# Kernel tuning notes

Measured on AMD Instinct MI355X. Metric: run time of the kernel, lower is better.

Reference implementation:

```python
import jax, jax.numpy as jnp
import numpy as np

NEG_INF = -1000000000.0
B, S, E, H = 2, 2048, 1024, 16
HD = E // H


def setup_inputs() -> dict:
    key = jax.random.key(0)
    ks = jax.random.split(key, 5)
    sd = 1.0 / np.sqrt(E)
    return {
        "x": jax.random.normal(ks[0], (B, S, E), dtype=jnp.float32),
        "Wqkv": jax.random.normal(ks[1], (3 * E, E), dtype=jnp.float32) * sd,
        "bqkv": jax.random.normal(ks[2], (3 * E,), dtype=jnp.float32) * sd,
        "Wout": jax.random.normal(ks[3], (E, E), dtype=jnp.float32) * sd,
        "bout": jax.random.normal(ks[4], (E,), dtype=jnp.float32) * sd,
    }


def reference(x, Wqkv, bqkv, Wout, bout):
    # qkv projection (torch Linear: x @ W.T + b)
    qkv = x @ Wqkv.T + bqkv                      # [B, S, 3E]
    qkv = qkv.reshape(B, S, H, 3 * HD).transpose(0, 2, 1, 3)  # [B, H, S, 3*hd]
    q, k, v = jnp.split(qkv, 3, axis=-1)          # each [B, H, S, hd]
    scaled = jnp.einsum('bhqd,bhkd->bhqk', q, k) / jnp.sqrt(jnp.float32(HD))
    # faithful to source: mask = tril(ones) * NEG_INF (lower triangle incl. diagonal gets -1e9)
    mask = jnp.tril(jnp.ones((S, S), dtype=jnp.float32)) * NEG_INF
    scaled = scaled + mask                        # broadcast over [B, H]
    attention = jax.nn.softmax(scaled, axis=-1)
    values = jnp.einsum('bhqk,bhkd->bhqd', attention, v)
    values = values.transpose(0, 2, 1, 3).reshape(B, S, E)
    out = values @ Wout.T + bout
    return out
```

## Files before the change

kernel.cpp:

```cpp
#include <hip/hip_runtime.h>
#include <hip/hip_bf16.h>
#include <math.h>

#define Bb 2
#define Ss 2048
#define Ee 1024
#define Hh 16
#define HDd 64
#define NEG_INF_F -1000000000.0f

typedef __attribute__((ext_vector_type(8))) short bfrag;
typedef __attribute__((ext_vector_type(4))) float ffrag;
typedef __attribute__((ext_vector_type(16))) float ffrag16;
typedef __attribute__((ext_vector_type(8))) unsigned short us8;

#define C1F 0.1803368801f

__device__ __forceinline__ unsigned short f2bf(float x) {
  unsigned u = __float_as_uint(x);
  u += 0x7fffu + ((u >> 16) & 1u);
  return (unsigned short)(u >> 16);
}
__device__ __forceinline__ float bf2f(unsigned short h) {
  return __uint_as_float(((unsigned)h) << 16);
}

__device__ __forceinline__ void async_copy16(void* lds, const void* g) {
  __builtin_amdgcn_global_load_lds(
      (const __attribute__((address_space(1))) unsigned int*)g,
      (__attribute__((address_space(3))) unsigned int*)lds, 16, 0, 0);
}

__global__ __launch_bounds__(256) void split_all(
    const float* __restrict__ x, unsigned short* __restrict__ xh,
    const float* __restrict__ wq, unsigned short* __restrict__ wqh,
    unsigned short* __restrict__ wql,
    const float* __restrict__ wo, unsigned short* __restrict__ woh,
    unsigned short* __restrict__ wol) {
  int bid = blockIdx.x;
  const float* in;
  unsigned short *hi, *lo;
  if (bid < 4096) { in = x; hi = xh; lo = nullptr; }
  else if (bid < 7168) { bid -= 4096; in = wq; hi = wqh; lo = wql; }
  else { bid -= 7168; in = wo; hi = woh; lo = wol; }
  const int idx = (bid * 256 + threadIdx.x) * 4;
  const float4 v = *(const float4*)(in + idx);
  unsigned short h0 = f2bf(v.x), h1 = f2bf(v.y), h2 = f2bf(v.z), h3 = f2bf(v.w);
  ushort4 hv = {h0, h1, h2, h3};
  *(ushort4*)(hi + idx) = hv;
  if (lo) {
    ushort4 lv = {f2bf(v.x - bf2f(h0)), f2bf(v.y - bf2f(h1)),
                  f2bf(v.z - bf2f(h2)), f2bf(v.w - bf2f(h3))};
    *(ushort4*)(lo + idx) = lv;
  }
}

__device__ __forceinline__ int gemm_slot(int row, int q) {
  return (row >> 1) * 8 + ((((row & 1) * 4) | q) ^ ((row >> 1) & 7));
}
__device__ __forceinline__ int slot_src_off(int slot, int ld) {
  const int dr = slot >> 3;
  const int idx8 = (slot & 7) ^ (dr & 7);
  const int row = dr * 2 + (idx8 >> 2);
  const int q = idx8 & 3;
  return row * ld + q * 8;
}

__global__ __launch_bounds__(256) void gemm_qkv(
    const unsigned short* __restrict__ Ah,
    const unsigned short* __restrict__ Bh, const unsigned short* __restrict__ Bl,
    const float* __restrict__ bias,
    unsigned short* __restrict__ q_h, unsigned short* __restrict__ k_h,
    unsigned short* __restrict__ vt_h) {
  __shared__ unsigned short sm[3 * 4096];
  const int tid = threadIdx.x;
  const int lane = tid & 63;
  const int w = tid >> 6;
  const int wm = w >> 1;
  const int wn = w & 1;
  const int l31 = lane & 31;
  const int e = lane >> 5;
  const int m0 = blockIdx.x * 128;
  const int n0 = blockIdx.y * 128;

  int coff[2], ldsb[2];
#pragma unroll
  for (int u = 0; u < 2; ++u) {
    const int slot = w * 128 + u * 64 + lane;
    coff[u] = slot_src_off(slot, 1024);
    ldsb[u] = (w * 128 + u * 64) * 8;
  }
  const unsigned short* srcs[3] = {
      Ah + (size_t)m0 * 1024, Bh + (size_t)n0 * 1024, Bl + (size_t)n0 * 1024};

  ffrag16 acc[2][2];
#pragma unroll
  for (int i = 0; i < 2; ++i)
#pragma unroll
    for (int j = 0; j < 2; ++j) acc[i][j] = (ffrag16)0.f;

  int ca[2][2], cb[2][2];
#pragma unroll
  for (int t = 0; t < 2; ++t)
#pragma unroll
    for (int h2 = 0; h2 < 2; ++h2) {
      ca[t][h2] = gemm_slot(wm * 64 + t * 32 + l31, h2 * 2 + e) * 8;
      cb[t][h2] = gemm_slot(wn * 64 + t * 32 + l31, h2 * 2 + e) * 8;
    }

  for (int k0 = 0; k0 < 1024; k0 += 32) {
    __syncthreads();
#pragma unroll
    for (int t = 0; t < 3; ++t)
#pragma unroll
      for (int u = 0; u < 2; ++u)
        async_copy16(&sm[t * 4096 + ldsb[u]], srcs[t] + coff[u] + k0);
    __syncthreads();

    bfrag ah[2][2], bhf[2][2], blf[2][2];
#pragma unroll
    for (int t = 0; t < 2; ++t)
#pragma unroll
      for (int h2 = 0; h2 < 2; ++h2) {
        ah[t][h2] = *(const bfrag*)&sm[0 * 4096 + ca[t][h2]];
        bhf[t][h2] = *(const bfrag*)&sm[1 * 4096 + cb[t][h2]];
        blf[t][h2] = *(const bfrag*)&sm[2 * 4096 + cb[t][h2]];
      }
#pragma unroll
    for (int mt = 0; mt < 2; ++mt)
#pragma unroll
      for (int nt = 0; nt < 2; ++nt)
#pragma unroll
        for (int h2 = 0; h2 < 2; ++h2) {
          acc[mt][nt] = __builtin_amdgcn_mfma_f32_32x32x16_bf16(
              ah[mt][h2], bhf[nt][h2], acc[mt][nt], 0, 0, 0);
          acc[mt][nt] = __builtin_amdgcn_mfma_f32_32x32x16_bf16(
              ah[mt][h2], blf[nt][h2], acc[mt][nt], 0, 0, 0);
        }
  }

#pragma unroll
  for (int nt = 0; nt < 2; ++nt) {
    const int n = n0 + wn * 64 + nt * 32 + l31;
    const float bv = bias[n];
    const int h = n / 192;
    const int c = n - h * 192;
    const int d = c & 63;
#pragma unroll
    for (int mt = 0; mt < 2; ++mt) {
      if (c >= 128) {
#pragma unroll
        for (int g = 0; g < 4; ++g) {
          const int m = m0 + wm * 64 + mt * 32 + g * 8 + e * 4;
          const int bidx = m >> 11;
          const int s = m & 2047;
          ushort4 hv4;
          unsigned short* ph = (unsigned short*)&hv4;
#pragma unroll
          for (int r = 0; r < 4; ++r)
            ph[r] = f2bf(acc[mt][nt][g * 4 + r] + bv);
          const size_t off =
              (size_t)(bidx * 16 + h) * (64 * 2048) + (size_t)d * 2048 + s;
          *(ushort4*)(vt_h + off) = hv4;
        }
      } else {
        const float scale = (c < 64) ? C1F : 1.0f;
        unsigned short* dh = (c < 64) ? q_h : k_h;
#pragma unroll
        for (int g = 0; g < 4; ++g)
#pragma unroll
          for (int r = 0; r < 4; ++r) {
            const int m = m0 + wm * 64 + mt * 32 + g * 8 + e * 4 + r;
            const int bidx = m >> 11;
            const int s = m & 2047;
            const size_t off =
                (size_t)(bidx * 16 + h) * (2048 * 64) + (size_t)s * 64 + d;
            dh[off] = f2bf((acc[mt][nt][g * 4 + r] + bv) * scale);
          }
      }
    }
  }
}

__global__ __launch_bounds__(256) void gemm_out2(
    const unsigned short* __restrict__ A,
    const unsigned short* __restrict__ Bh, const unsigned short* __restrict__ Bl,
    const float* __restrict__ bias, float* __restrict__ out) {
  __shared__ unsigned short sm[8192];
  const int tid = threadIdx.x;
  const int lane = tid & 63;
  const int w = tid >> 6;
  const int wm = w >> 1;
  const int wn = w & 1;
  const int l31 = lane & 31;
  const int e = lane >> 5;
  const int m0 = blockIdx.x * 128;
  const int n0 = blockIdx.y * 64;

  int acoff[2], aldsb[2];
#pragma unroll
  for (int u = 0; u < 2; ++u) {
    const int slot = w * 128 + u * 64 + lane;
    acoff[u] = slot_src_off(slot, 1024);
    aldsb[u] = (w * 128 + u * 64) * 8;
  }
  const int bslot = w * 64 + lane;
  const int bcoff = slot_src_off(bslot, 1024);
  const int bldsb = bslot * 8;

  const unsigned short* Ap  = A + (size_t)m0 * 1024;
  const unsigned short* Bph = Bh + (size_t)n0 * 1024;
  const unsigned short* Bpl = Bl + (size_t)n0 * 1024;

  ffrag16 acc[2];
  acc[0] = (ffrag16)0.f;
  acc[1] = (ffrag16)0.f;

  int ca[2][2], cb[2];
#pragma unroll
  for (int t = 0; t < 2; ++t)
#pragma unroll
    for (int h2 = 0; h2 < 2; ++h2)
      ca[t][h2] = gemm_slot(wm * 64 + t * 32 + l31, h2 * 2 + e) * 8;
#pragma unroll
  for (int h2 = 0; h2 < 2; ++h2)
    cb[h2] = gemm_slot(wn * 32 + l31, h2 * 2 + e) * 8;

  for (int k0 = 0; k0 < 1024; k0 += 32) {
    __syncthreads();
#pragma unroll
    for (int u = 0; u < 2; ++u)
      async_copy16(&sm[0 + aldsb[u]], Ap + acoff[u] + k0);
    async_copy16(&sm[4096 + bldsb], Bph + bcoff + k0);
    async_copy16(&sm[6144 + bldsb], Bpl + bcoff + k0);
    __syncthreads();

    bfrag ah[2][2], bhf[2], blf[2];
#pragma unroll
    for (int t = 0; t < 2; ++t)
#pragma unroll
      for (int h2 = 0; h2 < 2; ++h2)
        ah[t][h2] = *(const bfrag*)&sm[0 + ca[t][h2]];
#pragma unroll
    for (int h2 = 0; h2 < 2; ++h2) {
      bhf[h2] = *(const bfrag*)&sm[4096 + cb[h2]];
      blf[h2] = *(const bfrag*)&sm[6144 + cb[h2]];
    }
#pragma unroll
    for (int mt = 0; mt < 2; ++mt)
#pragma unroll
      for (int h2 = 0; h2 < 2; ++h2) {
        acc[mt] = __builtin_amdgcn_mfma_f32_32x32x16_bf16(
            ah[mt][h2], bhf[h2], acc[mt], 0, 0, 0);
        acc[mt] = __builtin_amdgcn_mfma_f32_32x32x16_bf16(
            ah[mt][h2], blf[h2], acc[mt], 0, 0, 0);
      }
  }

  const int n = n0 + wn * 32 + l31;
  const float bv = bias[n];
#pragma unroll
  for (int mt = 0; mt < 2; ++mt)
#pragma unroll
    for (int g = 0; g < 4; ++g)
#pragma unroll
      for (int r = 0; r < 4; ++r) {
        const int m = m0 + wm * 64 + mt * 32 + g * 8 + e * 4 + r;
        out[(size_t)m * 1024 + n] = acc[mt][g * 4 + r] + bv;
      }
}

__global__ __launch_bounds__(256, 4) void attn_2ph(
    const unsigned short* __restrict__ qh, const unsigned short* __restrict__ kh,
    const unsigned short* __restrict__ vth, unsigned short* __restrict__ vals) {
  __shared__ unsigned short sm[2 * 8192 + 4096];
  const int tid = threadIdx.x;
  const int lane = tid & 63;
  const int w = tid >> 6;
  const int l15 = lane & 15;
  const int quad = lane >> 4;
  const int bh = blockIdx.x;
  const int y = blockIdx.y;
  const size_t base = (size_t)bh * (Ss * HDd);
  const int b = bh >> 4;
  const int h = bh & 15;
  const int PB = 16384;

  const int c0 = w * 128 + lane;
  const int c1 = c0 + 64;
  const int r0 = c0 >> 3, r1 = c1 >> 3;
  const int s0 = ((c0 & 7) ^ (r0 & 7)) * 8;
  const int s1 = ((c1 & 7) ^ (r1 & 7)) * 8;
  const int koff0 = r0 * 64 + s0, koff1 = r1 * 64 + s1;
  const int voff0 = r0 * 2048 + s0, voff1 = r1 * 2048 + s1;
  const int ldsc0 = c0 * 8;
  const int ldsc1 = c1 * 8;

  bfrag vone;
#pragma unroll
  for (int j = 0; j < 8; ++j) vone[j] = (short)0x3F80;

  const bool fixw = (y == 0) && (w == 3);
  ffrag Vsum[4];
#pragma unroll
  for (int dt = 0; dt < 4; ++dt) Vsum[dt] = (ffrag)0.f;

  for (int ph = 0; ph < 2; ++ph) {
    const int ybk = ph ? (31 - y) : y;
    const int rb = 64 * ybk + 16 * w;

    bfrag Qf[2];
#pragma unroll
    for (int ks = 0; ks < 2; ++ks)
      Qf[ks] = *(const bfrag*)(qh + base + (size_t)(rb + l15) * 64 + ks * 32 + quad * 8);

    ffrag O[4], Oe;
#pragma unroll
    for (int dt = 0; dt < 4; ++dt) O[dt] = (ffrag)0.f;
    Oe = (ffrag)0.f;

    int cur = 0, nxt = 8192;
    {
      const unsigned short* kp = kh + base + ybk * 4096;
      const unsigned short* vp = vth + base + ybk * 64;
      async_copy16(&sm[cur + ldsc0], kp + koff0);
      async_copy16(&sm[cur + ldsc1], kp + koff1);
      async_copy16(&sm[cur + 4096 + ldsc0], vp + voff0);
      async_copy16(&sm[cur + 4096 + ldsc1], vp + voff1);
    }

    for (int kt = ybk; kt < 32; ++kt) {
      __syncthreads();
      if (kt + 1 < 32) {
        const unsigned short* kp = kh + base + (kt + 1) * 4096;
        const unsigned short* vp = vth + base + (kt + 1) * 64;
        async_copy16(&sm[nxt + ldsc0], kp + koff0);
        async_copy16(&sm[nxt + ldsc1], kp + koff1);
        async_copy16(&sm[nxt + 4096 + ldsc0], vp + voff0);
        async_copy16(&sm[nxt + 4096 + ldsc1], vp + voff1);
      }

      ffrag S[4];
#pragma unroll
      for (int nt = 0; nt < 4; ++nt) S[nt] = (ffrag)0.f;
#pragma unroll
      for (int nt = 0; nt < 4; ++nt) {
        const int krow = nt * 16 + l15;
#pragma unroll
        for (int ks = 0; ks < 2; ++ks) {
          const bfrag kbh =
              *(const bfrag*)&sm[cur + krow * 64 + ((ks * 4 + quad) ^ (krow & 7)) * 8];
          S[nt] = __builtin_amdgcn_mfma_f32_16x16x32_bf16(Qf[ks], kbh, S[nt], 0, 0, 0);
        }
      }

      const float CM = -1.442695041e9f;
      const bool partial = (kt == ybk);
#pragma unroll
      for (int nt = 0; nt < 4; ++nt) {
        const int key = nt * 16 + l15;
#pragma unroll
        for (int rp = 0; rp < 2; ++rp) {
          float t0 = S[nt][2 * rp];
          float t1 = S[nt][2 * rp + 1];
          if (partial) {
            const int jg = kt * 64 + key;
            const int ig = rb + quad * 4 + 2 * rp;
            if (jg <= ig) t0 += CM;
            if (jg <= ig + 1) t1 += CM;
          }
          float2 pf;
          pf.x = __builtin_amdgcn_exp2f(t0);
          pf.y = __builtin_amdgcn_exp2f(t1);
          const __hip_bfloat162 pb = __float22bfloat162_rn(pf);
          const unsigned short* pbs = (const unsigned short*)&pb;
          const int pr0 = w * 16 + quad * 4 + 2 * rp;
          sm[PB + pr0 * 64 + (((key >> 3) ^ (pr0 & 7)) * 8 + (key & 7))] = pbs[0];
          const int pr1 = pr0 + 1;
          sm[PB + pr1 * 64 + (((key >> 3) ^ (pr1 & 7)) * 8 + (key & 7))] = pbs[1];
        }
      }

#pragma unroll
      for (int ks = 0; ks < 2; ++ks) {
        const int prow = w * 16 + l15;
        const bfrag pA =
            *(const bfrag*)&sm[PB + prow * 64 + ((ks * 4 + quad) ^ (prow & 7)) * 8];
        Oe = __builtin_amdgcn_mfma_f32_16x16x32_bf16(pA, vone, Oe, 0, 0, 0);
#pragma unroll
        for (int dt = 0; dt < 4; ++dt) {
          const int vrow = dt * 16 + l15;
          const bfrag vbh =
              *(const bfrag*)&sm[cur + 4096 + vrow * 64 + ((ks * 4 + quad) ^ (vrow & 7)) * 8];
          O[dt] = __builtin_amdgcn_mfma_f32_16x16x32_bf16(pA, vbh, O[dt], 0, 0, 0);
          if (fixw && ph == 0)
            Vsum[dt] = __builtin_amdgcn_mfma_f32_16x16x32_bf16(vone, vbh, Vsum[dt], 0, 0, 0);
        }
      }
      const int t = cur; cur = nxt; nxt = t;
    }

#pragma unroll
    for (int r = 0; r < 4; ++r) {
      const float inv = 1.0f / Oe[r];
      const int s = rb + quad * 4 + r;
      const size_t rowoff = ((size_t)b * 2048 + s) * 1024 + h * 64;
#pragma unroll
      for (int dt = 0; dt < 4; ++dt) {
        float val = O[dt][r] * inv;
        if (fixw && ph == 1 && quad == 3 && r == 3)
          val = Vsum[dt][3] * (1.0f / 2048.0f);
        vals[rowoff + dt * 16 + l15] = f2bf(val);
      }
    }
    __syncthreads();
  }
}

extern "C" void kernel_launch(void* const* d_in, const int* in_sizes, int n_in,
                              void* d_out, int out_size, void* d_ws, size_t ws_size,
                              hipStream_t stream) {
  const float* x    = (const float*)d_in[0];
  const float* Wqkv = (const float*)d_in[1];
  const float* bqkv = (const float*)d_in[2];
  const float* Wout = (const float*)d_in[3];
  const float* bout = (const float*)d_in[4];
  float* out = (float*)d_out;
  char* wsb = (char*)d_ws;

  unsigned short* qhp  = (unsigned short*)d_ws;
  unsigned short* khp  = qhp + 1 * 4194304;
  unsigned short* vthp = qhp + 2 * 4194304;
  unsigned short* vals = qhp + 3 * 4194304;
  unsigned short* wqh  = (unsigned short*)(wsb + (48u << 20));
  unsigned short* wql  = (unsigned short*)(wsb + (54u << 20));
  unsigned short* woh  = (unsigned short*)(wsb + (60u << 20));
  unsigned short* wol  = (unsigned short*)(wsb + (62u << 20));
  unsigned short* xh   = (unsigned short*)d_out;

  dim3 blk(256);
  split_all<<<8192, blk, 0, stream>>>(x, xh, Wqkv, wqh, wql, Wout, woh, wol);
  gemm_qkv<<<dim3(32, 24), blk, 0, stream>>>(xh, wqh, wql, bqkv, qhp, khp, vthp);
  attn_2ph<<<dim3(32, 16), blk, 0, stream>>>(qhp, khp, vthp, vals);
  gemm_out2<<<dim3(32, 16), blk, 0, stream>>>(vals, woh, wol, bout, out);
}
```

Baseline: 202.6 us.

## Triple-buffer LDS in QKV and output GEMMs with async prefetch two tiles ahead

Replaces the load-then-sync loop in both projection GEMMs with a three-stage LDS ring buffer. Global-to-LDS async copies are issued two K-steps ahead and waited on with explicit vmcnt waitcnts plus a single barrier per step. This overlaps global memory latency with MFMA work and drops one of the two barriers per iteration. It triples shared memory per block, which can lower occupancy, and it relies on hand-coded waitcnt encodings matching the number of copies in flight.

```diff
diff --git a/kernel.cpp b/kernel.cpp
--- a/kernel.cpp
+++ b/kernel.cpp
@@ -15,6 +15,10 @@
 typedef __attribute__((ext_vector_type(8))) unsigned short us8;
 
 #define C1F 0.1803368801f
+
+#define WAIT_VM6 0x0F76
+#define WAIT_VM4 0x0F74
+#define WAIT_VM0 0x0F70
 
 __device__ __forceinline__ unsigned short f2bf(float x) {
   unsigned u = __float_as_uint(x);
@@ -72,7 +76,7 @@
     const float* __restrict__ bias,
     unsigned short* __restrict__ q_h, unsigned short* __restrict__ k_h,
     unsigned short* __restrict__ vt_h) {
-  __shared__ unsigned short sm[3 * 4096];
+  __shared__ unsigned short sm[3 * 12288];
   const int tid = threadIdx.x;
   const int lane = tid & 63;
   const int w = tid >> 6;
@@ -108,23 +112,40 @@
       cb[t][h2] = gemm_slot(wn * 64 + t * 32 + l31, h2 * 2 + e) * 8;
     }
 
-  for (int k0 = 0; k0 < 1024; k0 += 32) {
-    __syncthreads();
-#pragma unroll
-    for (int t = 0; t < 3; ++t)
-#pragma unroll
-      for (int u = 0; u < 2; ++u)
-        async_copy16(&sm[t * 4096 + ldsb[u]], srcs[t] + coff[u] + k0);
-    __syncthreads();
+#pragma unroll
+  for (int t = 0; t < 3; ++t)
+#pragma unroll
+    for (int u = 0; u < 2; ++u)
+      async_copy16(&sm[0 + t * 4096 + ldsb[u]], srcs[t] + coff[u] + 0);
+#pragma unroll
+  for (int t = 0; t < 3; ++t)
+#pragma unroll
+    for (int u = 0; u < 2; ++u)
+      async_copy16(&sm[12288 + t * 4096 + ldsb[u]], srcs[t] + coff[u] + 32);
+
+  int b0 = 0, b1 = 12288, b2 = 24576;
+  for (int k = 0; k < 32; ++k) {
+    if (k < 31) __builtin_amdgcn_s_waitcnt(WAIT_VM6);
+    else        __builtin_amdgcn_s_waitcnt(WAIT_VM0);
+    __builtin_amdgcn_s_barrier();
+    __builtin_amdgcn_sched_barrier(0);
+    if (k + 2 < 32) {
+      const int k0 = (k + 2) * 32;
+#pragma unroll
+      for (int t = 0; t < 3; ++t)
+#pragma unroll
+        for (int u = 0; u < 2; ++u)
+          async_copy16(&sm[b2 + t * 4096 + ldsb[u]], srcs[t] + coff[u] + k0);
+    }
 
     bfrag ah[2][2], bhf[2][2], blf[2][2];
 #pragma unroll
     for (int t = 0; t < 2; ++t)
 #pragma unroll
       for (int h2 = 0; h2 < 2; ++h2) {
-        ah[t][h2] = *(const bfrag*)&sm[0 * 4096 + ca[t][h2]];
-        bhf[t][h2] = *(const bfrag*)&sm[1 * 4096 + cb[t][h2]];
-        blf[t][h2] = *(const bfrag*)&sm[2 * 4096 + cb[t][h2]];
+        ah[t][h2] = *(const bfrag*)&sm[b0 + 0 + ca[t][h2]];
+        bhf[t][h2] = *(const bfrag*)&sm[b0 + 4096 + cb[t][h2]];
+        blf[t][h2] = *(const bfrag*)&sm[b0 + 8192 + cb[t][h2]];
       }
 #pragma unroll
     for (int mt = 0; mt < 2; ++mt)
@@ -137,6 +158,7 @@
           acc[mt][nt] = __builtin_amdgcn_mfma_f32_32x32x16_bf16(
               ah[mt][h2], blf[nt][h2], acc[mt][nt], 0, 0, 0);
         }
+    const int tb = b0; b0 = b1; b1 = b2; b2 = tb;
   }
 
 #pragma unroll
@@ -186,7 +208,7 @@
     const unsigned short* __restrict__ A,
     const unsigned short* __restrict__ Bh, const unsigned short* __restrict__ Bl,
     const float* __restrict__ bias, float* __restrict__ out) {
-  __shared__ unsigned short sm[8192];
+  __shared__ unsigned short sm[3 * 8192];
   const int tid = threadIdx.x;
   const int lane = tid & 63;
   const int w = tid >> 6;
@@ -226,25 +248,44 @@
   for (int h2 = 0; h2 < 2; ++h2)
     cb[h2] = gemm_slot(wn * 32 + l31, h2 * 2 + e) * 8;
 
-  for (int k0 = 0; k0 < 1024; k0 += 32) {
-    __syncthreads();
+  {
 #pragma unroll
     for (int u = 0; u < 2; ++u)
-      async_copy16(&sm[0 + aldsb[u]], Ap + acoff[u] + k0);
-    async_copy16(&sm[4096 + bldsb], Bph + bcoff + k0);
-    async_copy16(&sm[6144 + bldsb], Bpl + bcoff + k0);
-    __syncthreads();
+      async_copy16(&sm[0 + aldsb[u]], Ap + acoff[u] + 0);
+    async_copy16(&sm[0 + 4096 + bldsb], Bph + bcoff + 0);
+    async_copy16(&sm[0 + 6144 + bldsb], Bpl + bcoff + 0);
+#pragma unroll
+    for (int u = 0; u < 2; ++u)
+      async_copy16(&sm[8192 + aldsb[u]], Ap + acoff[u] + 32);
+    async_copy16(&sm[8192 + 4096 + bldsb], Bph + bcoff + 32);
+    async_copy16(&sm[8192 + 6144 + bldsb], Bpl + bcoff + 32);
+  }
+
+  int b0 = 0, b1 = 8192, b2 = 16384;
+  for (int k = 0; k < 32; ++k) {
+    if (k < 31) __builtin_amdgcn_s_waitcnt(WAIT_VM4);
+    else        __builtin_amdgcn_s_waitcnt(WAIT_VM0);
+    __builtin_amdgcn_s_barrier();
+    __builtin_amdgcn_sched_barrier(0);
+    if (k + 2 < 32) {
+      const int k0 = (k + 2) * 32;
+#pragma unroll
+      for (int u = 0; u < 2; ++u)
+        async_copy16(&sm[b2 + aldsb[u]], Ap + acoff[u] + k0);
+      async_copy16(&sm[b2 + 4096 + bldsb], Bph + bcoff + k0);
+      async_copy16(&sm[b2 + 6144 + bldsb], Bpl + bcoff + k0);
+    }
 
     bfrag ah[2][2], bhf[2], blf[2];
 #pragma unroll
     for (int t = 0; t < 2; ++t)
 #pragma unroll
       for (int h2 = 0; h2 < 2; ++h2)
-        ah[t][h2] = *(const bfrag*)&sm[0 + ca[t][h2]];
+        ah[t][h2] = *(const bfrag*)&sm[b0 + ca[t][h2]];
 #pragma unroll
     for (int h2 = 0; h2 < 2; ++h2) {
-      bhf[h2] = *(const bfrag*)&sm[4096 + cb[h2]];
-      blf[h2] = *(const bfrag*)&sm[6144 + cb[h2]];
+      bhf[h2] = *(const bfrag*)&sm[b0 + 4096 + cb[h2]];
+      blf[h2] = *(const bfrag*)&sm[b0 + 6144 + cb[h2]];
     }
 #pragma unroll
     for (int mt = 0; mt < 2; ++mt)
@@ -255,6 +296,7 @@
         acc[mt] = __builtin_amdgcn_mfma_f32_32x32x16_bf16(
             ah[mt][h2], blf[h2], acc[mt], 0, 0, 0);
       }
+    const int tb = b0; b0 = b1; b1 = b2; b2 = tb;
   }
 
   const int n = n0 + wn * 32 + l31;
```

Measured after the change: 204.3 us. No clear change (+0.9%).

## Triple-buffer QKV GEMM LDS tiles with async prefetch two steps ahead

Applied to the files above, without the earlier changes.

Replaces the two-barrier load-then-compute loop in the QKV projection GEMM with a three-stage LDS ring. Global-to-LDS async copies are issued two k-steps ahead, and an explicit vmcnt wait plus a single barrier is used per iteration. The goal is to overlap global memory latency with MFMA work. LDS use triples to 72KB per block, which may lower occupancy, and the hand-coded waitcnt values must match the number of outstanding loads.

```diff
diff --git a/kernel.cpp b/kernel.cpp
--- a/kernel.cpp
+++ b/kernel.cpp
@@ -15,6 +15,9 @@
 typedef __attribute__((ext_vector_type(8))) unsigned short us8;
 
 #define C1F 0.1803368801f
+
+#define WAIT_VM6   0x0F76
+#define WAIT_VM0   0x0F70
 
 __device__ __forceinline__ unsigned short f2bf(float x) {
   unsigned u = __float_as_uint(x);
@@ -72,7 +75,7 @@
     const float* __restrict__ bias,
     unsigned short* __restrict__ q_h, unsigned short* __restrict__ k_h,
     unsigned short* __restrict__ vt_h) {
-  __shared__ unsigned short sm[3 * 4096];
+  __shared__ unsigned short sm[3 * 12288];
   const int tid = threadIdx.x;
   const int lane = tid & 63;
   const int w = tid >> 6;
@@ -108,23 +111,40 @@
       cb[t][h2] = gemm_slot(wn * 64 + t * 32 + l31, h2 * 2 + e) * 8;
     }
 
-  for (int k0 = 0; k0 < 1024; k0 += 32) {
-    __syncthreads();
-#pragma unroll
-    for (int t = 0; t < 3; ++t)
-#pragma unroll
-      for (int u = 0; u < 2; ++u)
-        async_copy16(&sm[t * 4096 + ldsb[u]], srcs[t] + coff[u] + k0);
-    __syncthreads();
+#pragma unroll
+  for (int t = 0; t < 3; ++t)
+#pragma unroll
+    for (int u = 0; u < 2; ++u)
+      async_copy16(&sm[0 + t * 4096 + ldsb[u]], srcs[t] + coff[u] + 0);
+#pragma unroll
+  for (int t = 0; t < 3; ++t)
+#pragma unroll
+    for (int u = 0; u < 2; ++u)
+      async_copy16(&sm[12288 + t * 4096 + ldsb[u]], srcs[t] + coff[u] + 32);
+
+  int b0 = 0, b1 = 12288, b2 = 24576;
+  for (int k = 0; k < 32; ++k) {
+    if (k < 31) __builtin_amdgcn_s_waitcnt(WAIT_VM6);
+    else        __builtin_amdgcn_s_waitcnt(WAIT_VM0);
+    __builtin_amdgcn_s_barrier();
+    __builtin_amdgcn_sched_barrier(0);
+    if (k + 2 < 32) {
+      const int k0 = (k + 2) * 32;
+#pragma unroll
+      for (int t = 0; t < 3; ++t)
+#pragma unroll
+        for (int u = 0; u < 2; ++u)
+          async_copy16(&sm[b2 + t * 4096 + ldsb[u]], srcs[t] + coff[u] + k0);
+    }
 
     bfrag ah[2][2], bhf[2][2], blf[2][2];
 #pragma unroll
     for (int t = 0; t < 2; ++t)
 #pragma unroll
       for (int h2 = 0; h2 < 2; ++h2) {
-        ah[t][h2] = *(const bfrag*)&sm[0 * 4096 + ca[t][h2]];
-        bhf[t][h2] = *(const bfrag*)&sm[1 * 4096 + cb[t][h2]];
-        blf[t][h2] = *(const bfrag*)&sm[2 * 4096 + cb[t][h2]];
+        ah[t][h2] = *(const bfrag*)&sm[b0 + 0 + ca[t][h2]];
+        bhf[t][h2] = *(const bfrag*)&sm[b0 + 4096 + cb[t][h2]];
+        blf[t][h2] = *(const bfrag*)&sm[b0 + 8192 + cb[t][h2]];
       }
 #pragma unroll
     for (int mt = 0; mt < 2; ++mt)
@@ -137,6 +157,7 @@
           acc[mt][nt] = __builtin_amdgcn_mfma_f32_32x32x16_bf16(
               ah[mt][h2], blf[nt][h2], acc[mt][nt], 0, 0, 0);
         }
+    const int tb = b0; b0 = b1; b1 = b2; b2 = tb;
   }
 
 #pragma unroll
```

Result: no change. 203.6 us (+0.5%).
